# Optimization experiments

Measured on AMD Instinct MI355X. Metric: run time of the kernel, lower is better.

Reference implementation:

```python
import jax, jax.numpy as jnp
import numpy as np

# ---- static skeleton structure (SMPL 24-joint, 23-edge kinematic tree) ----
SMPL_EDGES = [[0,1],[0,2],[0,3],[1,4],[2,5],[3,6],[4,7],[5,8],[6,9],[7,10],
              [8,11],[9,12],[9,13],[9,14],[12,15],[13,16],[14,17],[16,18],
              [17,19],[18,20],[19,21],[20,22],[21,23]]
KERNEL, STRIDE, PAD, DIST = 15, 2, 7, 1

def _edge_dist(edges):
    E = len(edges)
    m = np.full((E, E), 1e6)
    np.fill_diagonal(m, 0.0)
    for i, a in enumerate(edges):
        for j, b in enumerate(edges):
            if i != j and set(a) & set(b):
                m[i, j] = 1.0
    for k in range(E):  # Floyd-Warshall on the edge adjacency graph
        m = np.minimum(m, m[:, k:k+1] + m[k:k+1, :])
    return m

def _find_neighbor(edges, d, n_global):
    m = _edge_dist(edges); E = len(edges)
    nb = [list(np.nonzero(m[i] <= d)[0]) for i in range(E)]
    gp = list(nb[0])  # edges near root edge (keeps deep-motion-editing's known quirk)
    g_ids = [E + k for k in range(n_global)]
    for i in gp:
        nb[i].extend(g_ids)
    for _ in range(n_global):
        nb.append(gp + g_ids)
    return nb

def _find_seqs(edges):
    deg = {}
    for a, b in edges:
        deg[a] = deg.get(a, 0) + 1
        deg[b] = deg.get(b, 0) + 1
    seqs = []
    def rec(j, seq):
        if deg.get(j, 0) > 2 and j != 0:
            seqs.append(seq); seq = []
        if deg.get(j, 0) == 1:
            seqs.append(seq); return
        for idx, (a, b) in enumerate(edges):
            if a == j:
                rec(b, seq + [idx])
    rec(0, [])
    return seqs

def _pooling(edges, last_pool, global_ids):
    pools, new_edges = [], []
    for seq in _find_seqs(edges):
        if last_pool:
            pools.append(seq); continue
        if len(seq) % 2 == 1:
            pools.append([seq[0]]); new_edges.append(edges[seq[0]]); seq = seq[1:]
        for i in range(0, len(seq), 2):
            pools.append([seq[i], seq[i+1]])
            new_edges.append([edges[seq[i]][0], edges[seq[i+1]][1]])
    pools.append(list(global_ids))
    return pools, new_edges

def _conv_mask(nb, in_per, out_per):
    N = len(nb)
    mask = np.zeros((N*out_per, N*in_per, 1), np.float32)
    for i, ns in enumerate(nb):
        for j in ns:
            mask[i*out_per:(i+1)*out_per, j*in_per:(j+1)*in_per, 0] = 1.0
    return mask

def _pool_matrix(pools, n_nodes, cpe):
    W = np.zeros((len(pools)*cpe, n_nodes*cpe), np.float32)
    c = np.arange(cpe)
    for i, grp in enumerate(pools):
        for j in grp:
            W[i*cpe + c, j*cpe + c] = 1.0 / len(grp)
    return W

E0 = len(SMPL_EDGES)
N0 = E0 + 2  # 23 edges + global position node + root-velocity node (the '+4' channels)
MASK0 = jnp.asarray(_conv_mask(_find_neighbor(SMPL_EDGES, DIST, 2), 4, 8))  # (200,100,1)
_pools0, EDGES1 = _pooling(SMPL_EDGES, False, [E0, E0 + 1])
P0 = jnp.asarray(_pool_matrix(_pools0, N0, 8))  # (112,200)
N1 = len(EDGES1) + 1
MASK1 = jnp.asarray(_conv_mask(_find_neighbor(EDGES1, DIST, 1), 8, 16))  # (224,112,1)
_pools1, _ = _pooling(EDGES1, True, [N1 - 1])
P1 = jnp.asarray(_pool_matrix(_pools1, N1, 16))  # (112,224)

IN0, OUT0 = 4 * N0, 8 * N0    # 100, 200
IN1, OUT1 = 8 * N1, 16 * N1   # 112, 224
B, T_IN = 64, 2047            # 2048 frames after zero-frame append


def _skel_conv(x, w, b, mask):
    # masked Conv1d (skeleton-sparse weights), stride 2, zero padding 7, k=15
    y = jax.lax.conv_general_dilated(x, w * mask, window_strides=(STRIDE,),
                                     padding=[(PAD, PAD)],
                                     dimension_numbers=('NCH', 'OIH', 'NCH'))
    return y + b[None, :, None]


def _forward(x, w0, b0, w1, b1):
    # x: (B, T, C); append one zero frame on time dim, then to (B, C, T+1)
    out = jnp.concatenate([x, jnp.zeros_like(x[:, :1, :])], axis=1)
    out = out.transpose(0, 2, 1)
    out = jax.nn.relu(jnp.einsum('pc,bct->bpt', P0, _skel_conv(out, w0, b0, MASK0)))
    out = jax.nn.relu(jnp.einsum('pc,bct->bpt', P1, _skel_conv(out, w1, b1, MASK1)))
    return out  # (B, 112, (T+1)//4)


def setup_inputs() -> dict:
    key = jax.random.key(0)
    k = jax.random.split(key, 5)
    s = 0.05
    return {
        'x':  jax.random.normal(k[0], (B, T_IN, IN0), jnp.float32),
        'w0': jax.random.normal(k[1], (OUT0, IN0, KERNEL), jnp.float32) * s,
        'b0': jax.random.normal(k[2], (OUT0,), jnp.float32) * s,
        'w1': jax.random.normal(k[3], (OUT1, IN1, KERNEL), jnp.float32) * s,
        'b1': jax.random.normal(k[4], (OUT1,), jnp.float32) * s,
    }


def reference(x, w0, b0, w1, b1):
    return _forward(x, w0, b0, w1, b1)
```

## Files before the change

kernel.cpp:

```cpp
#include <hip/hip_runtime.h>


#define OFF_A2  107520u
#define OFF_BF0 322560u
#define OFF_BF1 323008u

typedef unsigned int uint32;
typedef __attribute__((ext_vector_type(8))) short bs8;
typedef __attribute__((ext_vector_type(4))) float f32x4;
union U8 { uint4 u; bs8 s; };

__constant__ int c_pool0_len[14] = {2,2,2,2,1,2,2,1,2,2,1,2,2,2};
__constant__ int c_pool0_mem[14][2] = {{0,3},{6,9},{1,4},{7,10},{2,2},{5,8},{11,14},{12,12},
                                       {15,17},{19,21},{13,13},{16,18},{20,22},{23,24}};
__constant__ unsigned c_nbm0[25] = {
 0x180000Fu,0x1800017u,0x1800027u,0x1800049u,0x92u,0x124u,0x248u,0x490u,
 0x3920u,0x240u,0x480u,0x7900u,0xB900u,0x13900u,0x4800u,0x29000u,
 0x52000u,0xA8000u,0x150000u,0x2A0000u,0x540000u,0x280000u,0x500000u,
 0x180000Fu,0x180000Fu
};
__constant__ int c_pool1_len[7] = {2,2,2,1,3,3,1};
__constant__ int c_pool1_mem[7][3] = {{0,1,1},{2,3,3},{4,5,5},{6,6,6},{7,8,9},{10,11,12},{13,13,13}};
__constant__ unsigned c_nbm1[14] = {
 0x2017u,0x2003u,0x201Du,0xCu,0x2035u,0x4F0u,0x4E0u,0x5E0u,
 0x380u,0x300u,0xCE0u,0x1C00u,0x1800u,0x2017u
};
__constant__ int c_g1p[7][2] = {{0,13},{1,3},{2,4},{5,6},{7,10},{8,11},{9,12}};
__constant__ int c_U1[7][8] = {
 {0,1,2,3,6,23,24,25},
 {3,4,6,7,9,10,25,25},
 {0,1,2,4,5,7,23,24},
 {2,5,8,11,12,13,14,25},
 {8,11,12,13,15,16,25,25},
 {12,13,15,16,17,18,19,20},
 {17,18,19,20,21,22,25,25}};
__constant__ int c_U2[7][8] = {
 {0,1,2,4,13,14,14,14},
 {0,2,3,4,13,14,14,14},
 {0,2,4,5,6,7,10,13},
 {5,6,7,10,14,14,14,14},
 {5,6,7,8,9,10,14,14},
 {5,6,7,10,11,12,14,14},
 {0,1,2,4,13,14,14,14}};
__constant__ unsigned c_pk1a[7] = {0xC0301000u,0xC8483018u,0xB8281000u,0x70604010u,
                                   0xC8786040u,0x98887860u,0xC8A89888u};
__constant__ unsigned c_pk1b[7] = {0xC8B81808u,0xC8503820u,0xC0382008u,0xC8685828u,
                                   0xC8806858u,0xA0908068u,0xC8B0A090u};
__constant__ unsigned c_pk2[7][2] = {
 {0x40201000u,0xE0E0E0D0u},{0x40302000u,0xE0E0E0D0u},{0x50402000u,0xD0A07060u},
 {0xA0706050u,0xE0E0E0E0u},{0x80706050u,0xE0E0A090u},{0xA0706050u,0xE0E0C0B0u},
 {0x40201000u,0xE0E0E0D0u}};

__device__ __forceinline__ uint32 f2bf(float v) {
  uint32 u = __float_as_uint(v);
  return (u + 0x7fffu + ((u >> 16) & 1u)) >> 16;
}

__global__ void prep_fused_weights(const float* __restrict__ w0, const float* __restrict__ b0,
                                   const float* __restrict__ w1, const float* __restrict__ b1,
                                   char* __restrict__ wsb) {
  int t = blockIdx.x * blockDim.x + threadIdx.x;
  if (t < 6720) {
    int lane = t & 63;
    int r = t >> 6;
    int k = r % 15, g = r / 15;
    int m = lane & 15, h = lane >> 4;
    int pool = (m < 8) ? c_g1p[g][0] : c_g1p[g][1];
    int c = m & 7;
    int L = c_pool0_len[pool];
    float inv = 1.f / (float)L;
    uint32 us[8];
#pragma unroll
    for (int j = 0; j < 8; ++j) {
      int node = c_U1[g][2 * h + (j >> 2)];
      int ci = j & 3;
      float v = 0.f;
      if (node < 25) {
        for (int jj = 0; jj < L; ++jj) {
          int mem = c_pool0_mem[pool][jj];
          if ((c_nbm0[mem] >> node) & 1u)
            v += w0[(mem * 8 + c) * 1500 + (node * 4 + ci) * 15 + k];
        }
        v *= inv;
      }
      us[j] = f2bf(v);
    }
    uint4 o = make_uint4(us[0] | (us[1] << 16), us[2] | (us[3] << 16),
                         us[4] | (us[5] << 16), us[6] | (us[7] << 16));
    reinterpret_cast<uint4*>(wsb)[t] = o;
  } else if (t < 6720 + 13440) {
    int t2 = t - 6720;
    int lane = t2 & 63;
    int r = t2 >> 6;
    int k = r % 15;
    int r2 = r / 15;
    int ks = r2 & 1, p = r2 >> 1;
    int c = lane & 15, h = lane >> 4;
    int node = c_U2[p][ks * 4 + h];
    int L = c_pool1_len[p];
    float inv = 1.f / (float)L;
    uint32 us[8];
#pragma unroll
    for (int j = 0; j < 8; ++j) {
      float v = 0.f;
      if (node < 14) {
        for (int jj = 0; jj < L; ++jj) {
          int mem = c_pool1_mem[p][jj];
          if ((c_nbm1[mem] >> node) & 1u)
            v += w1[(mem * 16 + c) * 1680 + (node * 8 + j) * 15 + k];
        }
        v *= inv;
      }
      us[j] = f2bf(v);
    }
    uint4 o = make_uint4(us[0] | (us[1] << 16), us[2] | (us[3] << 16),
                         us[4] | (us[5] << 16), us[6] | (us[7] << 16));
    reinterpret_cast<uint4*>(wsb + OFF_A2)[t2] = o;
  } else if (t < 6720 + 13440 + 112) {
    int p = t - (6720 + 13440);
    int i = p >> 3, c = p & 7;
    int L = c_pool0_len[i];
    float v = 0.f;
    for (int jj = 0; jj < L; ++jj) v += b0[c_pool0_mem[i][jj] * 8 + c];
    reinterpret_cast<float*>(wsb + OFF_BF0)[p] = v / (float)L;
  } else if (t < 6720 + 13440 + 224) {
    int p = t - (6720 + 13440 + 112);
    int i = p >> 4, c = p & 15;
    int L = c_pool1_len[i];
    float v = 0.f;
    for (int jj = 0; jj < L; ++jj) v += b1[c_pool1_mem[i][jj] * 16 + c];
    reinterpret_cast<float*>(wsb + OFF_BF1)[p] = v / (float)L;
  }
}

__global__ __launch_bounds__(896, 4) void conv_fused(const float* __restrict__ x,
                                                     const char* __restrict__ wsb,
                                                     float* __restrict__ out) {
  __shared__ __align__(16) unsigned char lds[301 * 256];
  unsigned char* const xs = lds;
  unsigned char* const ys = lds;
  const int tid = threadIdx.x;
  const int lane = tid & 63;
  const int w = tid >> 6;
  const int g = (w < 7) ? w : (w - 7);
  const int half = (w < 7) ? 0 : 1;
  const int m16 = lane & 15, h = lane >> 4;
  const int b = blockIdx.y;
  const int t0 = blockIdx.x << 6;
  const int f0y = 2 * t0 - 7;
  const int g0x = 4 * t0 - 21;

  const float* __restrict__ xb = x + (size_t)b * (2047 * 100);
  float4 rg[9];
#pragma unroll
  for (int i = 0; i < 9; ++i) {
    rg[i] = make_float4(0.f, 0.f, 0.f, 0.f);
    int e = tid + i * 896;
    if (e < 7525) {
      int f = e / 25, q = e - f * 25;
      int gt = g0x + f;
      if ((unsigned)gt < 2047u)
        rg[i] = *reinterpret_cast<const float4*>(xb + gt * 100 + 4 * q);
    }
  }
  for (int e = tid; e < 301; e += 896)
    *reinterpret_cast<uint2*>(xs + e * 256 + (200u ^ (((e >> 1) & 15) << 3))) =
        make_uint2(0u, 0u);
#pragma unroll
  for (int i = 0; i < 9; ++i) {
    int e = tid + i * 896;
    if (e < 7525) {
      int f = e / 25, q = e - f * 25;
      uint2 wv = make_uint2(f2bf(rg[i].x) | (f2bf(rg[i].y) << 16),
                            f2bf(rg[i].z) | (f2bf(rg[i].w) << 16));
      *reinterpret_cast<uint2*>(xs + f * 256 + ((q * 8) ^ (((f >> 1) & 15) << 3))) = wv;
    }
  }
  const uint4* __restrict__ A1p = reinterpret_cast<const uint4*>(wsb) + g * 960 + lane;
  U8 aw[15];
#pragma unroll
  for (int k = 0; k < 15; ++k) aw[k].u = A1p[k * 64];
  const int pa = c_g1p[g][0], pb = c_g1p[g][1];
  const int chbase = (h < 2) ? (pa * 8 + 4 * h) : (pb * 8 + 4 * (h - 2));
  const float4 bv0 = *reinterpret_cast<const float4*>(wsb + OFF_BF0 + chbase * 4);
  __syncthreads();

  const uint32 offA = (c_pk1a[g] >> (8 * h)) & 255u;
  const uint32 offB = (c_pk1b[g] >> (8 * h)) & 255u;
  f32x4 acc1[5];
#pragma unroll
  for (int q = 0; q < 5; ++q) acc1[q] = (f32x4)0.f;
  if (half == 0) {
#pragma unroll
    for (int k = 0; k < 15; ++k) {
      const uint32 sw = (uint32)(((m16 + (k >> 1)) & 15) << 3);
      const uint32 a0 = offA ^ sw, a1o = offB ^ sw;
      const unsigned char* base = xs + (2 * m16 + k) * 256;
#pragma unroll
      for (int nt = 0; nt < 5; ++nt) {
        uint2 lo = *reinterpret_cast<const uint2*>(base + nt * 8192 + a0);
        uint2 hi = *reinterpret_cast<const uint2*>(base + nt * 8192 + a1o);
        U8 bfr; bfr.u = make_uint4(lo.x, lo.y, hi.x, hi.y);
        acc1[nt] = __builtin_amdgcn_mfma_f32_16x16x32_bf16(aw[k].s, bfr.s, acc1[nt], 0, 0, 0);
      }
    }
  } else {
#pragma unroll
    for (int k = 0; k < 15; ++k) {
      const uint32 sw = (uint32)(((m16 + (k >> 1)) & 15) << 3);
      const uint32 a0 = offA ^ sw, a1o = offB ^ sw;
      const unsigned char* base = xs + (2 * m16 + k) * 256 + 5 * 8192;
#pragma unroll
      for (int nt = 0; nt < 4; ++nt) {
        uint2 lo = *reinterpret_cast<const uint2*>(base + nt * 8192 + a0);
        uint2 hi = *reinterpret_cast<const uint2*>(base + nt * 8192 + a1o);
        U8 bfr; bfr.u = make_uint4(lo.x, lo.y, hi.x, hi.y);
        acc1[nt] = __builtin_amdgcn_mfma_f32_16x16x32_bf16(aw[k].s, bfr.s, acc1[nt], 0, 0, 0);
      }
    }
  }

  const uint4* __restrict__ A2p =
      reinterpret_cast<const uint4*>(wsb + OFF_A2) + g * 1920 + lane;
#pragma unroll
  for (int k = 0; k < 15; ++k) aw[k].u = A2p[k * 64];
  const float4 bv1 = *reinterpret_cast<const float4*>(wsb + OFF_BF1 + (g * 16 + 4 * h) * 4);
  __syncthreads();

  const int ntN = (half == 0) ? 5 : 4;
  const int ntB = half * 5;
#pragma unroll 5
  for (int ntl = 0; ntl < ntN; ++ntl) {
    int row = (ntB + ntl) * 16 + m16;
    int fy = f0y + row;
    float o0 = fmaxf(acc1[ntl][0] + bv0.x, 0.f);
    float o1 = fmaxf(acc1[ntl][1] + bv0.y, 0.f);
    float o2 = fmaxf(acc1[ntl][2] + bv0.z, 0.f);
    float o3 = fmaxf(acc1[ntl][3] + bv0.w, 0.f);
    uint2 wpk = make_uint2(f2bf(o0) | (f2bf(o1) << 16), f2bf(o2) | (f2bf(o3) << 16));
    if ((unsigned)fy >= 1024u) wpk = make_uint2(0u, 0u);
    *reinterpret_cast<uint2*>(ys + row * 256 +
        (((uint32)(chbase * 2)) ^ (((row >> 1) & 7) << 4))) = wpk;
  }
  for (int e = tid; e < 144; e += 896)
    *reinterpret_cast<uint4*>(ys + e * 256 + (224u ^ (((e >> 1) & 7) << 4))) =
        make_uint4(0u, 0u, 0u, 0u);
  __syncthreads();

  f32x4 acc2[2];
  acc2[0] = (f32x4)0.f; acc2[1] = (f32x4)0.f;
  const uint32 htoff = (uint32)(half * 2 * 8192);
  {
    const uint32 noff = (c_pk2[g][0] >> (8 * h)) & 255u;
#pragma unroll
    for (int k = 0; k < 15; ++k) {
      const uint32 sw = (uint32)(((m16 + (k >> 1)) & 7) << 4);
      const unsigned char* base = ys + (2 * m16 + k) * 256 + (noff ^ sw) + htoff;
      U8 b0f, b1f;
      b0f.u = *reinterpret_cast<const uint4*>(base);
      b1f.u = *reinterpret_cast<const uint4*>(base + 8192);
      acc2[0] = __builtin_amdgcn_mfma_f32_16x16x32_bf16(aw[k].s, b0f.s, acc2[0], 0, 0, 0);
      acc2[1] = __builtin_amdgcn_mfma_f32_16x16x32_bf16(aw[k].s, b1f.s, acc2[1], 0, 0, 0);
    }
  }
#pragma unroll
  for (int k = 0; k < 15; ++k) aw[k].u = A2p[(15 + k) * 64];
  {
    const uint32 noff = (c_pk2[g][1] >> (8 * h)) & 255u;
#pragma unroll
    for (int k = 0; k < 15; ++k) {
      const uint32 sw = (uint32)(((m16 + (k >> 1)) & 7) << 4);
      const unsigned char* base = ys + (2 * m16 + k) * 256 + (noff ^ sw) + htoff;
      U8 b0f, b1f;
      b0f.u = *reinterpret_cast<const uint4*>(base);
      b1f.u = *reinterpret_cast<const uint4*>(base + 8192);
      acc2[0] = __builtin_amdgcn_mfma_f32_16x16x32_bf16(aw[k].s, b0f.s, acc2[0], 0, 0, 0);
      acc2[1] = __builtin_amdgcn_mfma_f32_16x16x32_bf16(aw[k].s, b1f.s, acc2[1], 0, 0, 0);
    }
  }

#pragma unroll
  for (int n = 0; n < 2; ++n) {
    int nt_s2 = half * 2 + n;
    size_t obase = ((size_t)b * 112 + g * 16 + 4 * h) * 512 + t0 + nt_s2 * 16 + m16;
    out[obase]        = fmaxf(acc2[n][0] + bv1.x, 0.f);
    out[obase + 512]  = fmaxf(acc2[n][1] + bv1.y, 0.f);
    out[obase + 1024] = fmaxf(acc2[n][2] + bv1.z, 0.f);
    out[obase + 1536] = fmaxf(acc2[n][3] + bv1.w, 0.f);
  }
}

extern "C" void kernel_launch(void* const* d_in, const int* in_sizes, int n_in,
                              void* d_out, int out_size, void* d_ws, size_t ws_size,
                              hipStream_t stream) {
  const float* x  = (const float*)d_in[0];
  const float* w0 = (const float*)d_in[1];
  const float* b0 = (const float*)d_in[2];
  const float* w1 = (const float*)d_in[3];
  const float* b1 = (const float*)d_in[4];
  char* wsb = (char*)d_ws;
  float* out = (float*)d_out;

  prep_fused_weights<<<80, 256, 0, stream>>>(w0, b0, w1, b1, wsb);
  conv_fused<<<dim3(8, 64), 896, 0, stream>>>(x, wsb, out);
}
```

Before: 56.42 us.

## Repack stage-2 weights for 32x32 MFMA and cut stage-2 waves to eight

Stage 2 of the fused skeleton conv is restructured. Groups 0-5 now use 32x32x16 bf16 MFMA tiles, with weights repacked in the prep kernel into a new 32-channel, node-pair layout, and only neighbour node pairs that are actually needed are iterated. Group 6 keeps the old 16x16 path. Stage 2 now runs on 8 of the 14 waves instead of all 14, and the goal is fewer MFMA issues and fewer redundant LDS reads for zero neighbour blocks. In exchange the other waves sit idle during stage 2, the prep kernel does more work, and the output stores are less coalesced per wave.

```diff
diff --git a/kernel.cpp b/kernel.cpp
--- a/kernel.cpp
+++ b/kernel.cpp
@@ -4,10 +4,12 @@
 #define OFF_A2  107520u
 #define OFF_BF0 322560u
 #define OFF_BF1 323008u
+#define OFF_A2Q 323456u
 
 typedef unsigned int uint32;
 typedef __attribute__((ext_vector_type(8))) short bs8;
 typedef __attribute__((ext_vector_type(4))) float f32x4;
+typedef __attribute__((ext_vector_type(16))) float f32x16;
 union U8 { uint4 u; bs8 s; };
 
 __constant__ int c_pool0_len[14] = {2,2,2,2,1,2,2,1,2,2,1,2,2,2};
@@ -50,6 +52,11 @@
  {0x40201000u,0xE0E0E0D0u},{0x40302000u,0xE0E0E0D0u},{0x50402000u,0xD0A07060u},
  {0xA0706050u,0xE0E0E0E0u},{0x80706050u,0xE0E0A090u},{0xA0706050u,0xE0E0C0B0u},
  {0x40201000u,0xE0E0E0D0u}};
+__constant__ int c_q2steps[3] = {3, 4, 4};
+__constant__ int c_q2n[3][4][2] = {
+ {{0,1},{2,3},{4,13},{13,13}},
+ {{0,2},{4,5},{6,7},{10,13}},
+ {{5,6},{7,8},{9,10},{11,12}}};
 
 __device__ __forceinline__ uint32 f2bf(float v) {
   uint32 u = __float_as_uint(v);
@@ -130,6 +137,35 @@
     float v = 0.f;
     for (int jj = 0; jj < L; ++jj) v += b1[c_pool1_mem[i][jj] * 16 + c];
     reinterpret_cast<float*>(wsb + OFF_BF1)[p] = v / (float)L;
+  } else if (t < 6720 + 13440 + 224 + 11520) {
+    int tq = t - (6720 + 13440 + 224);
+    int lane = tq & 63;
+    int r = tq >> 6;
+    int k = r % 15;
+    int r2 = r / 15;
+    int s = r2 & 3, q = r2 >> 2;
+    int ch = q * 32 + (lane & 31);
+    int p = ch >> 4, c = ch & 15;
+    int node = c_q2n[q][s][lane >> 5];
+    int L = c_pool1_len[p];
+    float inv = 1.f / (float)L;
+    uint32 us[8];
+#pragma unroll
+    for (int j = 0; j < 8; ++j) {
+      float v = 0.f;
+      if (node < 14 && s < c_q2steps[q]) {
+        for (int jj = 0; jj < L; ++jj) {
+          int mem = c_pool1_mem[p][jj];
+          if ((c_nbm1[mem] >> node) & 1u)
+            v += w1[(mem * 16 + c) * 1680 + (node * 8 + j) * 15 + k];
+        }
+        v *= inv;
+      }
+      us[j] = f2bf(v);
+    }
+    uint4 o = make_uint4(us[0] | (us[1] << 16), us[2] | (us[3] << 16),
+                         us[4] | (us[5] << 16), us[6] | (us[7] << 16));
+    reinterpret_cast<uint4*>(wsb + OFF_A2Q)[tq] = o;
   }
 }
 
@@ -141,9 +177,9 @@
   unsigned char* const ys = lds;
   const int tid = threadIdx.x;
   const int lane = tid & 63;
-  const int w = tid >> 6;
-  const int g = (w < 7) ? w : (w - 7);
-  const int half = (w < 7) ? 0 : 1;
+  const int wv = tid >> 6;
+  const int g = (wv < 7) ? wv : (wv - 7);
+  const int half = (wv < 7) ? 0 : 1;
   const int m16 = lane & 15, h = lane >> 4;
   const int b = blockIdx.y;
   const int t0 = blockIdx.x << 6;
@@ -171,9 +207,9 @@
     int e = tid + i * 896;
     if (e < 7525) {
       int f = e / 25, q = e - f * 25;
-      uint2 wv = make_uint2(f2bf(rg[i].x) | (f2bf(rg[i].y) << 16),
+      uint2 w2 = make_uint2(f2bf(rg[i].x) | (f2bf(rg[i].y) << 16),
                             f2bf(rg[i].z) | (f2bf(rg[i].w) << 16));
-      *reinterpret_cast<uint2*>(xs + f * 256 + ((q * 8) ^ (((f >> 1) & 15) << 3))) = wv;
+      *reinterpret_cast<uint2*>(xs + f * 256 + ((q * 8) ^ (((f >> 1) & 15) << 3))) = w2;
     }
   }
   const uint4* __restrict__ A1p = reinterpret_cast<const uint4*>(wsb) + g * 960 + lane;
@@ -219,12 +255,6 @@
       }
     }
   }
-
-  const uint4* __restrict__ A2p =
-      reinterpret_cast<const uint4*>(wsb + OFF_A2) + g * 1920 + lane;
-#pragma unroll
-  for (int k = 0; k < 15; ++k) aw[k].u = A2p[k * 64];
-  const float4 bv1 = *reinterpret_cast<const float4*>(wsb + OFF_BF1 + (g * 16 + 4 * h) * 4);
   __syncthreads();
 
   const int ntN = (half == 0) ? 5 : 4;
@@ -247,46 +277,88 @@
         make_uint4(0u, 0u, 0u, 0u);
   __syncthreads();
 
-  f32x4 acc2[2];
-  acc2[0] = (f32x4)0.f; acc2[1] = (f32x4)0.f;
-  const uint32 htoff = (uint32)(half * 2 * 8192);
-  {
-    const uint32 noff = (c_pk2[g][0] >> (8 * h)) & 255u;
-#pragma unroll
-    for (int k = 0; k < 15; ++k) {
-      const uint32 sw = (uint32)(((m16 + (k >> 1)) & 7) << 4);
-      const unsigned char* base = ys + (2 * m16 + k) * 256 + (noff ^ sw) + htoff;
-      U8 b0f, b1f;
-      b0f.u = *reinterpret_cast<const uint4*>(base);
-      b1f.u = *reinterpret_cast<const uint4*>(base + 8192);
-      acc2[0] = __builtin_amdgcn_mfma_f32_16x16x32_bf16(aw[k].s, b0f.s, acc2[0], 0, 0, 0);
-      acc2[1] = __builtin_amdgcn_mfma_f32_16x16x32_bf16(aw[k].s, b1f.s, acc2[1], 0, 0, 0);
-    }
-  }
-#pragma unroll
-  for (int k = 0; k < 15; ++k) aw[k].u = A2p[(15 + k) * 64];
-  {
-    const uint32 noff = (c_pk2[g][1] >> (8 * h)) & 255u;
-#pragma unroll
-    for (int k = 0; k < 15; ++k) {
-      const uint32 sw = (uint32)(((m16 + (k >> 1)) & 7) << 4);
-      const unsigned char* base = ys + (2 * m16 + k) * 256 + (noff ^ sw) + htoff;
-      U8 b0f, b1f;
-      b0f.u = *reinterpret_cast<const uint4*>(base);
-      b1f.u = *reinterpret_cast<const uint4*>(base + 8192);
-      acc2[0] = __builtin_amdgcn_mfma_f32_16x16x32_bf16(aw[k].s, b0f.s, acc2[0], 0, 0, 0);
-      acc2[1] = __builtin_amdgcn_mfma_f32_16x16x32_bf16(aw[k].s, b1f.s, acc2[1], 0, 0, 0);
-    }
-  }
-
-#pragma unroll
-  for (int n = 0; n < 2; ++n) {
-    int nt_s2 = half * 2 + n;
-    size_t obase = ((size_t)b * 112 + g * 16 + 4 * h) * 512 + t0 + nt_s2 * 16 + m16;
-    out[obase]        = fmaxf(acc2[n][0] + bv1.x, 0.f);
-    out[obase + 512]  = fmaxf(acc2[n][1] + bv1.y, 0.f);
-    out[obase + 1024] = fmaxf(acc2[n][2] + bv1.z, 0.f);
-    out[obase + 1536] = fmaxf(acc2[n][3] + bv1.w, 0.f);
+  if (wv < 8) {
+    const int q2 = wv & 3;
+    const int h2 = wv >> 2;
+    if (q2 < 3) {
+      const int colL = h2 * 32 + (lane & 31);
+      const int nodeSel = lane >> 5;
+      const uint4* __restrict__ A2Qp =
+          reinterpret_cast<const uint4*>(wsb + OFF_A2Q) + (q2 * 4 * 15) * 64 + lane;
+      f32x16 acc = (f32x16)0.f;
+      const int nsteps = c_q2steps[q2];
+#pragma unroll 1
+      for (int s = 0; s < nsteps; ++s) {
+        U8 aw2[15];
+#pragma unroll
+        for (int k = 0; k < 15; ++k) aw2[k].u = A2Qp[(s * 15 + k) * 64];
+        const uint32 noff = (uint32)(c_q2n[q2][s][nodeSel] * 16);
+#pragma unroll
+        for (int k = 0; k < 15; ++k) {
+          int row = 2 * colL + k;
+          U8 bf;
+          bf.u = *reinterpret_cast<const uint4*>(
+              ys + row * 256 + (noff ^ (uint32)(((row >> 1) & 7) << 4)));
+          acc = __builtin_amdgcn_mfma_f32_32x32x16_bf16(aw2[k].s, bf.s, acc, 0, 0, 0);
+        }
+      }
+      const float* __restrict__ BF1f = reinterpret_cast<const float*>(wsb + OFF_BF1);
+      const int t = t0 + colL;
+#pragma unroll
+      for (int r = 0; r < 16; ++r) {
+        int chRow = (r & 3) + 8 * (r >> 2) + 4 * nodeSel;
+        int ch = q2 * 32 + chRow;
+        float bvv = BF1f[ch];
+        out[((size_t)b * 112 + ch) * 512 + t] = fmaxf(acc[r] + bvv, 0.f);
+      }
+    } else {
+      const uint4* __restrict__ A2p =
+          reinterpret_cast<const uint4*>(wsb + OFF_A2) + 6 * 1920 + lane;
+      const float4 bv1 =
+          *reinterpret_cast<const float4*>(wsb + OFF_BF1 + (6 * 16 + 4 * h) * 4);
+      U8 aw3[15];
+#pragma unroll
+      for (int k = 0; k < 15; ++k) aw3[k].u = A2p[k * 64];
+      f32x4 acc2[2];
+      acc2[0] = (f32x4)0.f; acc2[1] = (f32x4)0.f;
+      const uint32 htoff = (uint32)(h2 * 16384);
+      {
+        const uint32 noff = (c_pk2[6][0] >> (8 * h)) & 255u;
+#pragma unroll
+        for (int k = 0; k < 15; ++k) {
+          const uint32 sw = (uint32)(((m16 + (k >> 1)) & 7) << 4);
+          const unsigned char* base = ys + (2 * m16 + k) * 256 + (noff ^ sw) + htoff;
+          U8 b0f, b1f;
+          b0f.u = *reinterpret_cast<const uint4*>(base);
+          b1f.u = *reinterpret_cast<const uint4*>(base + 8192);
+          acc2[0] = __builtin_amdgcn_mfma_f32_16x16x32_bf16(aw3[k].s, b0f.s, acc2[0], 0, 0, 0);
+          acc2[1] = __builtin_amdgcn_mfma_f32_16x16x32_bf16(aw3[k].s, b1f.s, acc2[1], 0, 0, 0);
+        }
+      }
+#pragma unroll
+      for (int k = 0; k < 15; ++k) aw3[k].u = A2p[(15 + k) * 64];
+      {
+        const uint32 noff = (c_pk2[6][1] >> (8 * h)) & 255u;
+#pragma unroll
+        for (int k = 0; k < 15; ++k) {
+          const uint32 sw = (uint32)(((m16 + (k >> 1)) & 7) << 4);
+          const unsigned char* base = ys + (2 * m16 + k) * 256 + (noff ^ sw) + htoff;
+          U8 b0f, b1f;
+          b0f.u = *reinterpret_cast<const uint4*>(base);
+          b1f.u = *reinterpret_cast<const uint4*>(base + 8192);
+          acc2[0] = __builtin_amdgcn_mfma_f32_16x16x32_bf16(aw3[k].s, b0f.s, acc2[0], 0, 0, 0);
+          acc2[1] = __builtin_amdgcn_mfma_f32_16x16x32_bf16(aw3[k].s, b1f.s, acc2[1], 0, 0, 0);
+        }
+      }
+#pragma unroll
+      for (int n = 0; n < 2; ++n) {
+        size_t obase = ((size_t)b * 112 + 96 + 4 * h) * 512 + t0 + h2 * 32 + n * 16 + m16;
+        out[obase]        = fmaxf(acc2[n][0] + bv1.x, 0.f);
+        out[obase + 512]  = fmaxf(acc2[n][1] + bv1.y, 0.f);
+        out[obase + 1024] = fmaxf(acc2[n][2] + bv1.z, 0.f);
+        out[obase + 1536] = fmaxf(acc2[n][3] + bv1.w, 0.f);
+      }
+    }
   }
 }
 
@@ -301,6 +373,6 @@
   char* wsb = (char*)d_ws;
   float* out = (float*)d_out;
 
-  prep_fused_weights<<<80, 256, 0, stream>>>(w0, b0, w1, b1, wsb);
+  prep_fused_weights<<<125, 256, 0, stream>>>(w0, b0, w1, b1, wsb);
   conv_fused<<<dim3(8, 64), 896, 0, stream>>>(x, wsb, out);
 }
```

Result: slower. 60.22 us (+6.7%).
